# Performance work log

Measured on AMD Instinct MI355X. Metric: run time of the kernel, lower is better.

Reference implementation:

```python
import jax, jax.numpy as jnp
import numpy as np

MAX_DIST = 10
FP_PENALTY = 2.0


def _min_dist_to(mask, BIG):
    """Per-position distance to the nearest True in mask along axis 1.

    mask: [B, S] bool. Returns int32 [B, S]; BIG where the row has no True.
    Replaces the O(B*S_switch^2) Python loops with two cummax scans.
    """
    B, S = mask.shape
    idx = jnp.arange(S, dtype=jnp.int32)
    def one_side(m):
        last = jax.lax.cummax(jnp.where(m, idx, jnp.int32(-BIG)), axis=1)
        return idx - last  # distance to nearest True at or before each position
    d_fwd = one_side(mask)
    d_bwd = jnp.flip(one_side(jnp.flip(mask, axis=1)), axis=1)
    return jnp.minimum(jnp.minimum(d_fwd, d_bwd), BIG)


def setup_inputs() -> dict:
    key = jax.random.key(0)
    k1, k2 = jax.random.split(key)
    B, S, C = 256, 32768, 3
    logits = jax.random.normal(k1, (B, S, C), dtype=jnp.float32)
    labels = jax.random.randint(k2, (B, S), 0, 3, dtype=jnp.int32)
    distance_weights = jnp.array(
        [1.0, 0.99, 0.95, 0.9, 0.85, 0.8, 0.75, 0.7, 0.65, 0.6, 0.55], jnp.float32)
    class_weights = jnp.array([1.0, 10.0, 10.0], jnp.float32)
    return {"logits": logits, "labels": labels,
            "distance_weights": distance_weights, "class_weights": class_weights}


def reference(logits, labels, distance_weights, class_weights):
    B, S, C = logits.shape
    BIG = 2 * S

    valid = labels != -100
    safe_labels = jnp.where(valid, labels, 0)

    # weighted CE, reduction='none', ignore_index=-100
    logp = jax.nn.log_softmax(logits, axis=-1)
    nll = -jnp.take_along_axis(logp, safe_labels[..., None], axis=-1)[..., 0]
    ce = jnp.where(valid, nll * class_weights[safe_labels], 0.0)

    switch = (labels == 1) | (labels == 2)          # true switch positions
    preds = jnp.argmax(logits, axis=-1)
    pred_switch = (preds == 1) | (preds == 2)       # predicted switch positions

    d_to_true = _min_dist_to(switch, BIG)           # nearest true switch per position
    d_to_pred = _min_dist_to(pred_switch, BIG)      # nearest predicted switch per position

    validf = valid.astype(ce.dtype)

    # proximity bonus at valid predicted-switch positions near a true switch
    n_w = distance_weights.shape[0]
    w = jnp.take(distance_weights, jnp.clip(d_to_true, 0, n_w - 1))
    bonus_mask = pred_switch & valid & (d_to_true <= MAX_DIST)
    bonus = jnp.where(bonus_mask, ce * w * 0.5, 0.0)

    # double CE at valid true switches far from every predicted switch
    # (torch code skips this entirely when the row has no predicted switch)
    has_pred = jnp.any(pred_switch, axis=1, keepdims=True)
    double_mask = switch & valid & has_pred & (d_to_pred > MAX_DIST)
    ce = jnp.where(double_mask, ce * 2.0, ce) - bonus

    masked = ce * validf
    fp = pred_switch.astype(ce.dtype) * (1.0 - switch.astype(ce.dtype)) * validf * FP_PENALTY
    total = masked + fp
    return total.sum() / jnp.maximum(validf.sum(), 1.0)
```

## Files before the change

### kernel.cpp

```cpp
#include <hip/hip_runtime.h>
#include <stdint.h>

#define MAX_DIST 10
#define FP_PENALTY 2.0f
#define CHUNK 4096
#define NT 256
#define ITERS (CHUNK / NT)
#define UF 4
#define NW64 (CHUNK / 64)
#define NDW (2 * NW64 + 2)

__global__ __launch_bounds__(NT, 8) void pal_main(
    const float* __restrict__ logits, const int* __restrict__ labels,
    const float* __restrict__ dw, const float* __restrict__ cw,
    double* __restrict__ blk_base, double* __restrict__ blk_extra,
    int* __restrict__ blk_valid, int* __restrict__ blk_haspred,
    int S, int chunks_per_row)
{
    __shared__ float ce_lds[CHUNK];
    __shared__ unsigned int swb[NDW];
    __shared__ unsigned int psb[NDW];
    __shared__ float tbl[12];
    __shared__ float rb[NT / 64], rex[NT / 64];
    __shared__ int rv[NT / 64], rfp[NT / 64], rp[NT / 64];

    const int t = threadIdx.x;
    const int wave = t >> 6, lane = t & 63;
    const int blk = blockIdx.x;
    const int row = blk / chunks_per_row;
    const int ck  = blk % chunks_per_row;
    const int s0  = ck * CHUNK;
    const long long rowbase = (long long)row * S;

    if (t < 12) tbl[t] = (t < 11) ? 0.5f * dw[t] : 0.0f;
    const float cw0 = cw[0], cw1 = cw[1], cw2 = cw[2];

    int svc = 0, sfp = 0;
    unsigned long long sanyp = 0ull;

    for (int j0 = 0; j0 < ITERS; j0 += UF) {
        int   lblv[UF];
        float l0v[UF], l1v[UF], l2v[UF];
        #pragma unroll
        for (int u = 0; u < UF; ++u) {
            const long long g = rowbase + s0 + (j0 + u) * NT + t;
            lblv[u] = labels[g];
            const float* lp = logits + g * 3;
            l0v[u] = lp[0]; l1v[u] = lp[1]; l2v[u] = lp[2];
        }
        #pragma unroll
        for (int u = 0; u < UF; ++u) {
            const int r = (j0 + u) * NT + t;
            const int lbl = lblv[u];
            const float l0 = l0v[u], l1 = l1v[u], l2 = l2v[u];

            int pred = 0; float best = l0;
            if (l1 > best) { best = l1; pred = 1; }
            if (l2 > best) { best = l2; pred = 2; }

            const bool valid = (lbl != -100);
            const int sl = valid ? lbl : 0;
            const float a = (pred == 0) ? l1 : l0;
            const float b = (pred == 2) ? l1 : l2;
            const float esum = 1.0f + __expf(a - best) + __expf(b - best);
            const float lse = best + __logf(esum);
            const float lt  = (sl == 0) ? l0 : (sl == 1 ? l1 : l2);
            const float cwv = (sl == 0) ? cw0 : (sl == 1 ? cw1 : cw2);
            ce_lds[r] = valid ? (lse - lt) * cwv : 0.0f;

            const bool sw = (lbl == 1) || (lbl == 2);
            const bool ps = (pred == 1) || (pred == 2);
            const unsigned long long bs = __ballot(sw ? 1 : 0);
            const unsigned long long bp = __ballot(ps ? 1 : 0);
            const unsigned long long bv = __ballot(valid ? 1 : 0);
            svc += (int)__popcll(bv);
            sfp += (int)__popcll(bp & ~bs & bv);
            sanyp |= bp;
            if (lane == 0) {
                const int W = r >> 6;
                swb[2 * W + 1] = (unsigned)bs; swb[2 * W + 2] = (unsigned)(bs >> 32);
                psb[2 * W + 1] = (unsigned)bp; psb[2 * W + 2] = (unsigned)(bp >> 32);
            }
        }
    }

    if (wave == 0) {
        bool sw = false, ps = false;
        int s = -1;
        if (lane < 10) s = s0 - 10 + lane;
        else if (lane >= 32 && lane < 42) s = s0 + CHUNK + (lane - 32);
        if (s >= 0 && s < S) {
            const long long g = rowbase + s;
            const int lbl = labels[g];
            const float* lp = logits + g * 3;
            const float l0 = lp[0], l1 = lp[1], l2 = lp[2];
            int pred = 0; float best = l0;
            if (l1 > best) { best = l1; pred = 1; }
            if (l2 > best) { best = l2; pred = 2; }
            sw = (lbl == 1) || (lbl == 2);
            ps = (pred == 1) || (pred == 2);
        }
        const unsigned long long bs = __ballot(sw ? 1 : 0);
        const unsigned long long bp = __ballot(ps ? 1 : 0);
        if (lane == 0) {
            swb[0] = (unsigned)((bs & 0x3FFull) << 22);
            psb[0] = (unsigned)((bp & 0x3FFull) << 22);
            swb[NDW - 1] = (unsigned)((bs >> 32) & 0x3FFull);
            psb[NDW - 1] = (unsigned)((bp >> 32) & 0x3FFull);
        }
    }
    __syncthreads();

    float base_acc = 0.0f, extra_acc = 0.0f;
    const int sh = (t + 22) & 31;
    const int wbase = (t + 22) >> 5;

    #pragma unroll 4
    for (int j = 0; j < ITERS; ++j) {
        const unsigned s0w = swb[wbase + j * 8], s1w = swb[wbase + j * 8 + 1];
        const unsigned p0w = psb[wbase + j * 8], p1w = psb[wbase + j * 8 + 1];
        const unsigned swin = __builtin_amdgcn_alignbit(s1w, s0w, sh);
        const unsigned pwin = __builtin_amdgcn_alignbit(p1w, p0w, sh);
        const float ce = ce_lds[t + j * NT];

        const bool sw_self = (swin >> 10) & 1u;
        const bool ps_self = (pwin >> 10) & 1u;
        const bool npnear  = (pwin & 0x1FFFFFu) == 0u;

        const unsigned low10 = swin & 0x3FFu;
        const unsigned up10  = (swin >> 11) & 0x3FFu;
        const int ddown = __clz((low10 << 21) | 0x100000u);
        const int dup   = __ffs(up10 | 0x400u);
        int dt = min(ddown, dup);
        dt = sw_self ? 0 : dt;

        const float f = ps_self ? tbl[dt] : 0.0f;
        base_acc += ce * (1.0f - f);
        extra_acc += (sw_self && npnear) ? ce : 0.0f;
    }

    for (int off = 32; off; off >>= 1) {
        base_acc  += __shfl_down(base_acc, off);
        extra_acc += __shfl_down(extra_acc, off);
    }
    if (lane == 0) {
        rb[wave]  = base_acc;
        rex[wave] = extra_acc;
        rv[wave]  = svc;
        rfp[wave] = sfp;
        rp[wave]  = (sanyp != 0ull) ? 1 : 0;
    }
    __syncthreads();
    if (t == 0) {
        double bsum = 0.0, esum = 0.0; int vs = 0, fps = 0, ap = 0;
        for (int i = 0; i < NT / 64; ++i) {
            bsum += rb[i]; esum += rex[i]; vs += rv[i]; fps += rfp[i]; ap |= rp[i];
        }
        blk_base[blk]    = bsum + (double)FP_PENALTY * (double)fps;
        blk_extra[blk]   = esum;
        blk_valid[blk]   = vs;
        blk_haspred[blk] = ap;
    }
}

__global__ __launch_bounds__(NT) void pal_finish(
    const double* __restrict__ blk_base, const double* __restrict__ blk_extra,
    const int* __restrict__ blk_valid, const int* __restrict__ blk_haspred,
    int nrows, int chunks_per_row, float* __restrict__ out)
{
    const int t = threadIdx.x;
    double bsum = 0.0, esum = 0.0;
    long long vsum = 0;
    for (int r = t; r < nrows; r += NT) {
        int hp = 0; double e = 0.0;
        for (int c = 0; c < chunks_per_row; ++c) {
            const int i = r * chunks_per_row + c;
            bsum += blk_base[i];
            e    += blk_extra[i];
            hp   |= blk_haspred[i];
            vsum += blk_valid[i];
        }
        if (hp) esum += e;
    }
    __shared__ double sb[NT], se[NT];
    __shared__ long long sv[NT];
    sb[t] = bsum; se[t] = esum; sv[t] = vsum;
    __syncthreads();
    for (int off = NT / 2; off; off >>= 1) {
        if (t < off) { sb[t] += sb[t + off]; se[t] += se[t + off]; sv[t] += sv[t + off]; }
        __syncthreads();
    }
    if (t == 0) {
        const double tot = sb[0] + se[0];
        double denom = (double)sv[0];
        if (denom < 1.0) denom = 1.0;
        out[0] = (float)(tot / denom);
    }
}

extern "C" void kernel_launch(void* const* d_in, const int* in_sizes, int n_in,
                              void* d_out, int out_size, void* d_ws, size_t ws_size,
                              hipStream_t stream)
{
    const float* logits = (const float*)d_in[0];
    const int*   labels = (const int*)d_in[1];
    const float* dw     = (const float*)d_in[2];
    const float* cw     = (const float*)d_in[3];

    const int S = 32768;
    const int Brows = in_sizes[1] / S;
    const int CPR = S / CHUNK;
    const int nblk = Brows * CPR;

    double* blk_base    = (double*)d_ws;
    double* blk_extra   = blk_base + nblk;
    int*    blk_valid   = (int*)(blk_extra + nblk);
    int*    blk_haspred = blk_valid + nblk;

    pal_main<<<nblk, NT, 0, stream>>>(logits, labels, dw, cw,
                                      blk_base, blk_extra, blk_valid, blk_haspred,
                                      S, CPR);
    pal_finish<<<1, NT, 0, stream>>>(blk_base, blk_extra, blk_valid, blk_haspred,
                                     Brows, CPR, (float*)d_out);
}
```

Measured before the change: 36.70 us.

## Assign contiguous 16-element runs per thread with vector loads and register-held CE

Each thread now processes 16 contiguous positions, loading labels and logits with int4/float4 vector loads instead of strided scalar loads. CE values stay in registers instead of being staged through a 16KB LDS buffer, and switch/pred bitmasks are built per thread as 16-bit words in LDS, which removes the per-element wave ballots. Neighbour windows come from just three LDS reads per thread. This cuts LDS traffic and load instruction count but raises register pressure, and launch bounds are lowered to 4 blocks per CU.

```diff
diff --git a/kernel.cpp b/kernel.cpp
--- a/kernel.cpp
+++ b/kernel.cpp
@@ -5,24 +5,22 @@
 #define FP_PENALTY 2.0f
 #define CHUNK 4096
 #define NT 256
-#define ITERS (CHUNK / NT)
-#define UF 4
-#define NW64 (CHUNK / 64)
-#define NDW (2 * NW64 + 2)
-
-__global__ __launch_bounds__(NT, 8) void pal_main(
+#define PPT (CHUNK / NT)
+#define NG 4
+#define GP 4
+
+__global__ __launch_bounds__(NT, 4) void pal_main(
     const float* __restrict__ logits, const int* __restrict__ labels,
     const float* __restrict__ dw, const float* __restrict__ cw,
     double* __restrict__ blk_base, double* __restrict__ blk_extra,
     int* __restrict__ blk_valid, int* __restrict__ blk_haspred,
     int S, int chunks_per_row)
 {
-    __shared__ float ce_lds[CHUNK];
-    __shared__ unsigned int swb[NDW];
-    __shared__ unsigned int psb[NDW];
+    __shared__ unsigned short swb[NT + 2];
+    __shared__ unsigned short psb[NT + 2];
     __shared__ float tbl[12];
     __shared__ float rb[NT / 64], rex[NT / 64];
-    __shared__ int rv[NT / 64], rfp[NT / 64], rp[NT / 64];
+    __shared__ int rvfp[NT / 64], rp[NT / 64];
 
     const int t = threadIdx.x;
     const int wave = t >> 6, lane = t & 63;
@@ -31,28 +29,36 @@
     const int ck  = blk % chunks_per_row;
     const int s0  = ck * CHUNK;
     const long long rowbase = (long long)row * S;
+    const long long pbase = rowbase + s0 + (long long)t * PPT;
 
     if (t < 12) tbl[t] = (t < 11) ? 0.5f * dw[t] : 0.0f;
     const float cw0 = cw[0], cw1 = cw[1], cw2 = cw[2];
 
-    int svc = 0, sfp = 0;
-    unsigned long long sanyp = 0ull;
-
-    for (int j0 = 0; j0 < ITERS; j0 += UF) {
-        int   lblv[UF];
-        float l0v[UF], l1v[UF], l2v[UF];
+    int4   lb[NG];
+    float4 x0[NG], x1[NG], x2[NG];
+    #pragma unroll
+    for (int g = 0; g < NG; ++g) {
+        lb[g] = *(const int4*)(labels + pbase + g * GP);
+        const float* lp = logits + (pbase + g * GP) * 3;
+        x0[g] = *(const float4*)(lp);
+        x1[g] = *(const float4*)(lp + 4);
+        x2[g] = *(const float4*)(lp + 8);
+    }
+    __builtin_amdgcn_sched_barrier(0);
+
+    float ce[PPT];
+    unsigned swm = 0u, psm = 0u, vvm = 0u;
+    #pragma unroll
+    for (int g = 0; g < NG; ++g) {
+        const float L[12] = { x0[g].x, x0[g].y, x0[g].z, x0[g].w,
+                              x1[g].x, x1[g].y, x1[g].z, x1[g].w,
+                              x2[g].x, x2[g].y, x2[g].z, x2[g].w };
+        const int lbl4[4] = { lb[g].x, lb[g].y, lb[g].z, lb[g].w };
         #pragma unroll
-        for (int u = 0; u < UF; ++u) {
-            const long long g = rowbase + s0 + (j0 + u) * NT + t;
-            lblv[u] = labels[g];
-            const float* lp = logits + g * 3;
-            l0v[u] = lp[0]; l1v[u] = lp[1]; l2v[u] = lp[2];
-        }
-        #pragma unroll
-        for (int u = 0; u < UF; ++u) {
-            const int r = (j0 + u) * NT + t;
-            const int lbl = lblv[u];
-            const float l0 = l0v[u], l1 = l1v[u], l2 = l2v[u];
+        for (int i = 0; i < GP; ++i) {
+            const int j = g * GP + i;
+            const int lbl = lbl4[i];
+            const float l0 = L[3*i], l1 = L[3*i+1], l2 = L[3*i+2];
 
             int pred = 0; float best = l0;
             if (l1 > best) { best = l1; pred = 1; }
@@ -66,23 +72,17 @@
             const float lse = best + __logf(esum);
             const float lt  = (sl == 0) ? l0 : (sl == 1 ? l1 : l2);
             const float cwv = (sl == 0) ? cw0 : (sl == 1 ? cw1 : cw2);
-            ce_lds[r] = valid ? (lse - lt) * cwv : 0.0f;
-
-            const bool sw = (lbl == 1) || (lbl == 2);
-            const bool ps = (pred == 1) || (pred == 2);
-            const unsigned long long bs = __ballot(sw ? 1 : 0);
-            const unsigned long long bp = __ballot(ps ? 1 : 0);
-            const unsigned long long bv = __ballot(valid ? 1 : 0);
-            svc += (int)__popcll(bv);
-            sfp += (int)__popcll(bp & ~bs & bv);
-            sanyp |= bp;
-            if (lane == 0) {
-                const int W = r >> 6;
-                swb[2 * W + 1] = (unsigned)bs; swb[2 * W + 2] = (unsigned)(bs >> 32);
-                psb[2 * W + 1] = (unsigned)bp; psb[2 * W + 2] = (unsigned)(bp >> 32);
-            }
-        }
-    }
+            ce[j] = valid ? (lse - lt) * cwv : 0.0f;
+
+            swm |= ((lbl == 1) || (lbl == 2)) ? (1u << j) : 0u;
+            psm |= (pred != 0) ? (1u << j) : 0u;
+            vvm |= valid ? (1u << j) : 0u;
+        }
+    }
+    swb[t + 1] = (unsigned short)swm;
+    psb[t + 1] = (unsigned short)psm;
+    const int vfp = __popc(vvm) | (__popc(psm & ~swm & vvm) << 16);
+    const bool anyp = (psm != 0u);
 
     if (wave == 0) {
         bool sw = false, ps = false;
@@ -103,29 +103,28 @@
         const unsigned long long bs = __ballot(sw ? 1 : 0);
         const unsigned long long bp = __ballot(ps ? 1 : 0);
         if (lane == 0) {
-            swb[0] = (unsigned)((bs & 0x3FFull) << 22);
-            psb[0] = (unsigned)((bp & 0x3FFull) << 22);
-            swb[NDW - 1] = (unsigned)((bs >> 32) & 0x3FFull);
-            psb[NDW - 1] = (unsigned)((bp >> 32) & 0x3FFull);
+            swb[0] = (unsigned short)((bs & 0x3FFull) << 6);
+            psb[0] = (unsigned short)((bp & 0x3FFull) << 6);
+            swb[NT + 1] = (unsigned short)((bs >> 32) & 0x3FFull);
+            psb[NT + 1] = (unsigned short)((bp >> 32) & 0x3FFull);
         }
     }
     __syncthreads();
 
+    const unsigned slo = (unsigned)swb[t] | ((unsigned)swb[t + 1] << 16);
+    const unsigned shi = (unsigned)swb[t + 2];
+    const unsigned plo = (unsigned)psb[t] | ((unsigned)psb[t + 1] << 16);
+    const unsigned phi = (unsigned)psb[t + 2];
+
     float base_acc = 0.0f, extra_acc = 0.0f;
-    const int sh = (t + 22) & 31;
-    const int wbase = (t + 22) >> 5;
-
-    #pragma unroll 4
-    for (int j = 0; j < ITERS; ++j) {
-        const unsigned s0w = swb[wbase + j * 8], s1w = swb[wbase + j * 8 + 1];
-        const unsigned p0w = psb[wbase + j * 8], p1w = psb[wbase + j * 8 + 1];
-        const unsigned swin = __builtin_amdgcn_alignbit(s1w, s0w, sh);
-        const unsigned pwin = __builtin_amdgcn_alignbit(p1w, p0w, sh);
-        const float ce = ce_lds[t + j * NT];
+    #pragma unroll
+    for (int j = 0; j < PPT; ++j) {
+        const unsigned swin = __builtin_amdgcn_alignbit(shi, slo, j + 6) & 0x1FFFFFu;
+        const unsigned pwin = __builtin_amdgcn_alignbit(phi, plo, j + 6) & 0x1FFFFFu;
 
         const bool sw_self = (swin >> 10) & 1u;
         const bool ps_self = (pwin >> 10) & 1u;
-        const bool npnear  = (pwin & 0x1FFFFFu) == 0u;
+        const bool npnear  = (pwin == 0u);
 
         const unsigned low10 = swin & 0x3FFu;
         const unsigned up10  = (swin >> 11) & 0x3FFu;
@@ -135,26 +134,26 @@
         dt = sw_self ? 0 : dt;
 
         const float f = ps_self ? tbl[dt] : 0.0f;
-        base_acc += ce * (1.0f - f);
-        extra_acc += (sw_self && npnear) ? ce : 0.0f;
-    }
-
+        base_acc += ce[j] * (1.0f - f);
+        extra_acc += (sw_self && npnear) ? ce[j] : 0.0f;
+    }
+
+    float ba = base_acc, ea = extra_acc; int vf = vfp;
     for (int off = 32; off; off >>= 1) {
-        base_acc  += __shfl_down(base_acc, off);
-        extra_acc += __shfl_down(extra_acc, off);
-    }
+        ba += __shfl_down(ba, off);
+        ea += __shfl_down(ea, off);
+        vf += __shfl_down(vf, off);
+    }
+    const bool wave_any = __any(anyp ? 1 : 0);
     if (lane == 0) {
-        rb[wave]  = base_acc;
-        rex[wave] = extra_acc;
-        rv[wave]  = svc;
-        rfp[wave] = sfp;
-        rp[wave]  = (sanyp != 0ull) ? 1 : 0;
+        rb[wave] = ba; rex[wave] = ea; rvfp[wave] = vf; rp[wave] = wave_any ? 1 : 0;
     }
     __syncthreads();
     if (t == 0) {
         double bsum = 0.0, esum = 0.0; int vs = 0, fps = 0, ap = 0;
         for (int i = 0; i < NT / 64; ++i) {
-            bsum += rb[i]; esum += rex[i]; vs += rv[i]; fps += rfp[i]; ap |= rp[i];
+            bsum += rb[i]; esum += rex[i];
+            vs += rvfp[i] & 0xFFFF; fps += rvfp[i] >> 16; ap |= rp[i];
         }
         blk_base[blk]    = bsum + (double)FP_PENALTY * (double)fps;
         blk_extra[blk]   = esum;
```

New measurement: 35.39 us. 3.5% less time.
